# Kernel tuning notes

Measured on AMD Instinct MI355X. Metric: run time of the kernel, lower is better.

Reference implementation:

```python
import jax, jax.numpy as jnp
import numpy as np

# hparams (SpeechSplit-style, scaled up)
MAX_LEN_SEQ = 2048
MAX_LEN_PAD = 2560
MIN_LEN_SEG = 19
MAX_LEN_SEG = 32
MAX_NUM_SEG = MAX_LEN_SEQ // MIN_LEN_SEG + 1  # 108
B = 32
D = 80
S = MAX_LEN_SEG * 2  # 64 candidate interp positions per segment
N = B * MAX_NUM_SEG  # 3456


def setup_inputs() -> dict:
    key = jax.random.key(0)
    k1, k2, k3, k4 = jax.random.split(key, 4)
    x = jax.random.normal(k1, (B, MAX_LEN_PAD, D), dtype=jnp.float32)
    len_seq = jax.random.randint(k2, (B,), 0, MAX_LEN_SEQ, dtype=jnp.int32)
    scales_u = jax.random.uniform(k3, (N,), dtype=jnp.float32)  # uniform [0,1); +0.5 inside reference
    len_seg_raw = jax.random.randint(k4, (N, 1), 0, MAX_LEN_SEG - MIN_LEN_SEG, dtype=jnp.int32)
    return {"x": x, "len_seq": len_seq, "scales_u": scales_u, "len_seg_raw": len_seg_raw}


def reference(x, len_seq, scales_u, len_seg_raw):
    b, tx, d = x.shape
    # per-segment scaled time indices
    idx = jnp.arange(S, dtype=jnp.float32)[None, :]                     # (1, S)
    scales = scales_u + 0.5                                             # (N,) in [0.5, 1.5)
    idx_scaled = idx / scales[:, None]                                  # (N, S)
    idx_fl = jnp.floor(idx_scaled)
    lam = idx_scaled - idx_fl                                           # lerp weight (N, S)
    len_seg = len_seg_raw + MIN_LEN_SEG                                 # (N, 1) int
    idx_mask = idx_fl < (len_seg.astype(jnp.float32) - 1.0)             # within this segment
    # cumulative segment offsets per batch row
    offset = jnp.cumsum(len_seg.reshape(b, MAX_NUM_SEG), axis=-1)
    offset = jnp.pad(offset[:, :-1], ((0, 0), (1, 0))).reshape(-1, 1)   # (N, 1)
    idx_org = idx_fl + offset.astype(jnp.float32)                       # absolute source frame
    len_seq_rp = jnp.repeat(len_seq, MAX_NUM_SEG)                       # (N,)
    mask = idx_mask & (idx_org < (len_seq_rp - 1).astype(jnp.float32)[:, None])  # (N, S)

    mask_f = mask.reshape(-1)                                           # (N*S,)
    pos = jnp.cumsum(mask_f.astype(jnp.int32)) - 1                      # compacted position per element
    total = mask_f.astype(jnp.int32).sum()                              # total compacted rows

    # gather floor/ceil frames (index_1 = batch row of each flattened element)
    elem_batch = (jnp.arange(N * S, dtype=jnp.int32) // (MAX_NUM_SEG * S))
    i_fl = jnp.clip(idx_org.reshape(-1).astype(jnp.int32), 0, tx - 2)   # masked elems always in-range
    y_fl = x[elem_batch, i_fl]                                          # (N*S, D)
    y_cl = x[elem_batch, i_fl + 1]                                      # (N*S, D)
    lam_f = lam.reshape(-1, 1)
    y = (1.0 - lam_f) * y_fl + lam_f * y_cl                             # linear interp

    # boolean compaction via scatter into fixed-size buffer (masked-out rows dropped)
    write_pos = jnp.where(mask_f, pos, N * S)
    buf = jnp.zeros((N * S, d), x.dtype).at[write_pos].set(y, mode='drop')

    # reshape compacted stream to (b, total//b, d), trim/pad to MAX_LEN_PAD
    rows = total // b
    t = jnp.arange(MAX_LEN_PAD)
    gidx = jnp.arange(b)[:, None] * rows + t[None, :]                   # (b, MAX_LEN_PAD)
    valid = t[None, :] < rows
    out = jnp.where(valid[..., None], buf[jnp.clip(gidx, 0, N * S - 1)], 0.0)
    return out
```

## Files before the change

kernel.cpp:

```cpp
#include <hip/hip_runtime.h>
#include <hip/hip_bf16.h>

#define MAX_LEN_PAD 2560
#define MIN_LEN_SEG 19
#define MAX_NUM_SEG 108
#define B_ROWS      32
#define S_CAND      64
#define N_SEG       3456

#define WS_META      0
#define WS_SEGSTART  16
#define WS_SEGOFF    3504
#define WS_TABLE     8192

__global__ __launch_bounds__(576) void k1_scan(
    const int* __restrict__ len_seq, const float* __restrict__ scales_u,
    const int* __restrict__ len_seg_raw, int* __restrict__ ws)
{
    __shared__ int s_part[16];
    __shared__ int s_rowcum[B_ROWS];

    const int tid  = threadIdx.x;
    const int lane = tid & 63;
    const int wave = tid >> 6;
    const int brow = tid / 18;

    int v[6]; float sc[6];
    int sum = 0;
    #pragma unroll
    for (int j = 0; j < 6; ++j) {
        int k = tid * 6 + j;
        v[j]  = len_seg_raw[k] + MIN_LEN_SEG;
        sc[j] = scales_u[k];
        sum  += v[j];
    }

    int incl = sum;
    #pragma unroll
    for (int d = 1; d < 64; d <<= 1) {
        int o = __shfl_up(incl, d, 64);
        if (lane >= d) incl += o;
    }
    if (lane == 63) s_part[wave] = incl;
    __syncthreads();
    if (tid == 0) {
        int run = 0;
        #pragma unroll
        for (int w = 0; w < 9; ++w) { int p = s_part[w]; s_part[w] = run; run += p; }
    }
    __syncthreads();
    const int gbase = s_part[wave] + incl - sum;
    if (tid % 18 == 0) s_rowcum[brow] = gbase;
    __syncthreads();

    const int ls = len_seq[brow];
    const int rowc = s_rowcum[brow];
    int cnt[6]; int csum = 0;
    int* seg_off = ws + WS_SEGOFF;
    {
        int run = gbase;
        #pragma unroll
        for (int j = 0; j < 6; ++j) {
            int off = run - rowc;
            seg_off[tid * 6 + j] = off;
            run += v[j];
            float scale = sc[j] + 0.5f;
            int T = v[j] - 1;
            int lim = ls - 1 - off;
            if (lim < T) T = lim;
            float Tf = (float)T;
            int lo = 0, hi = S_CAND;
            while (lo < hi) {
                int mid = (lo + hi) >> 1;
                if (floorf((float)mid / scale) < Tf) lo = mid + 1; else hi = mid;
            }
            cnt[j] = lo; csum += lo;
        }
    }

    int cincl = csum;
    #pragma unroll
    for (int d = 1; d < 64; d <<= 1) {
        int o = __shfl_up(cincl, d, 64);
        if (lane >= d) cincl += o;
    }
    if (lane == 63) s_part[wave] = cincl;
    __syncthreads();
    if (tid == 0) {
        int run = 0;
        #pragma unroll
        for (int w = 0; w < 9; ++w) { int p = s_part[w]; s_part[w] = run; run += p; }
        int total = run;
        ws[WS_SEGSTART + N_SEG] = total;
        int rows = total / B_ROWS;
        int M = rows < MAX_LEN_PAD ? rows : MAX_LEN_PAD;
        ws[WS_META + 0] = rows;
        ws[WS_META + 1] = M;
    }
    __syncthreads();
    {
        int run = s_part[wave] + cincl - csum;
        int* seg_start = ws + WS_SEGSTART;
        #pragma unroll
        for (int j = 0; j < 6; ++j) { seg_start[tid * 6 + j] = run; run += cnt[j]; }
    }
}

__global__ __launch_bounds__(512) void k2_table(
    const float* __restrict__ scales_u, int* __restrict__ ws)
{
    const int n = blockIdx.x * 8 + (threadIdx.x >> 6);
    const int s = threadIdx.x & 63;
    const int rows = ws[WS_META + 0];
    if (rows <= 0) return;

    const int* seg_start = ws + WS_SEGSTART;
    int s0  = seg_start[n];
    int cnt = seg_start[n + 1] - s0;
    if (s >= cnt) return;

    float scale = scales_u[n] + 0.5f;
    int off = ws[WS_SEGOFF + n];
    int g = s0 + s;
    int b_out = g / rows;
    int t = g - b_out * rows;
    if (b_out < B_ROWS && t < MAX_LEN_PAD) {
        float q  = (float)s / scale;
        float fi = floorf(q);
        float lam = q - fi;
        int i_fl = (int)fi + off;
        if (i_fl > MAX_LEN_PAD - 2) i_fl = MAX_LEN_PAD - 2;
        int src = (n / MAX_NUM_SEG) * MAX_LEN_PAD + i_fl;
        ((int2*)(ws + WS_TABLE))[b_out * MAX_LEN_PAD + t] =
            make_int2(src, __float_as_int(lam));
    }
}

__global__ __launch_bounds__(640) void k3_gather(
    const float* __restrict__ x, const int* __restrict__ ws,
    float* __restrict__ out)
{
    const int M = ws[WS_META + 1];
    int flat = blockIdx.x * 640 + threadIdx.x;
    int r  = flat / 20;
    int q4 = flat - r * 20;
    int t  = r % MAX_LEN_PAD;

    float4 res = make_float4(0.f, 0.f, 0.f, 0.f);
    if (t < M) {
        int2 e = ((const int2*)(ws + WS_TABLE))[r];
        int src = e.x;
        float lam = __int_as_float(e.y);
        const float4* x4 = (const float4*)x;
        float4 a = x4[src * 20 + q4];
        float4 c = x4[src * 20 + 20 + q4];
        float om = 1.0f - lam;
        res.x = om * a.x + lam * c.x;
        res.y = om * a.y + lam * c.y;
        res.z = om * a.z + lam * c.z;
        res.w = om * a.w + lam * c.w;
    }
    ((float4*)out)[flat] = res;
}

extern "C" void kernel_launch(void* const* d_in, const int* in_sizes, int n_in,
                              void* d_out, int out_size, void* d_ws, size_t ws_size,
                              hipStream_t stream) {
    (void)in_sizes; (void)n_in; (void)out_size; (void)ws_size;
    const float* x           = (const float*)d_in[0];
    const int*   len_seq     = (const int*)d_in[1];
    const float* scales_u    = (const float*)d_in[2];
    const int*   len_seg_raw = (const int*)d_in[3];
    float* out = (float*)d_out;
    int*   ws  = (int*)d_ws;

    k1_scan<<<1, 576, 0, stream>>>(len_seq, scales_u, len_seg_raw, ws);
    k2_table<<<432, 512, 0, stream>>>(scales_u, ws);
    k3_gather<<<2560, 640, 0, stream>>>(x, ws, out);
}
```

Before: 90.87 us.

## Fuse interpolation table construction into single-block scan kernel

Merges the table-building kernel into the scan kernel. The scan runs in one 1024-thread block that keeps segment starts, offsets and scales in shared memory, then writes the gather table in 16-element chunks per thread. This removes a kernel launch and the workspace round-trip for segment metadata. The cost is that the whole table is written by a single workgroup, which limits parallelism and memory throughput for that phase.

```diff
diff --git a/kernel.cpp b/kernel.cpp
--- a/kernel.cpp
+++ b/kernel.cpp
@@ -8,31 +8,35 @@
 #define S_CAND      64
 #define N_SEG       3456
 
-#define WS_META      0
-#define WS_SEGSTART  16
-#define WS_SEGOFF    3504
-#define WS_TABLE     8192
+#define WS_META   0
+#define WS_TABLE  8192
 
-__global__ __launch_bounds__(576) void k1_scan(
+__global__ __launch_bounds__(1024) void k1_all(
     const int* __restrict__ len_seq, const float* __restrict__ scales_u,
     const int* __restrict__ len_seg_raw, int* __restrict__ ws)
 {
-    __shared__ int s_part[16];
-    __shared__ int s_rowcum[B_ROWS];
+    __shared__ int   s_part[16];
+    __shared__ int   s_rowcum[B_ROWS];
+    __shared__ int   s_misc[2];
+    __shared__ int   s_start[N_SEG + 1];
+    __shared__ int   s_off[N_SEG];
+    __shared__ float s_scale[N_SEG];
 
-    const int tid  = threadIdx.x;
-    const int lane = tid & 63;
-    const int wave = tid >> 6;
-    const int brow = tid / 18;
+    const int tid    = threadIdx.x;
+    const int lane   = tid & 63;
+    const int wave   = tid >> 6;
+    const bool active = tid < N_SEG / 6;
+    const int brow   = tid / 18;
 
-    int v[6]; float sc[6];
-    int sum = 0;
-    #pragma unroll
-    for (int j = 0; j < 6; ++j) {
-        int k = tid * 6 + j;
-        v[j]  = len_seg_raw[k] + MIN_LEN_SEG;
-        sc[j] = scales_u[k];
-        sum  += v[j];
+    int v[6]; float sc[6]; int sum = 0;
+    if (active) {
+        #pragma unroll
+        for (int j = 0; j < 6; ++j) {
+            int k = tid * 6 + j;
+            v[j]  = len_seg_raw[k] + MIN_LEN_SEG;
+            sc[j] = scales_u[k];
+            sum  += v[j];
+        }
     }
 
     int incl = sum;
@@ -46,23 +50,22 @@
     if (tid == 0) {
         int run = 0;
         #pragma unroll
-        for (int w = 0; w < 9; ++w) { int p = s_part[w]; s_part[w] = run; run += p; }
+        for (int w = 0; w < 16; ++w) { int p = s_part[w]; s_part[w] = run; run += p; }
     }
     __syncthreads();
     const int gbase = s_part[wave] + incl - sum;
-    if (tid % 18 == 0) s_rowcum[brow] = gbase;
+    if (active && (tid % 18 == 0)) s_rowcum[brow] = gbase;
     __syncthreads();
 
-    const int ls = len_seq[brow];
-    const int rowc = s_rowcum[brow];
-    int cnt[6]; int csum = 0;
-    int* seg_off = ws + WS_SEGOFF;
-    {
+    int cnt[6]; int csum = 0; int offv[6];
+    if (active) {
+        const int ls   = len_seq[brow];
+        const int rowc = s_rowcum[brow];
         int run = gbase;
         #pragma unroll
         for (int j = 0; j < 6; ++j) {
             int off = run - rowc;
-            seg_off[tid * 6 + j] = off;
+            offv[j] = off;
             run += v[j];
             float scale = sc[j] + 0.5f;
             int T = v[j] - 1;
@@ -89,50 +92,57 @@
     if (tid == 0) {
         int run = 0;
         #pragma unroll
-        for (int w = 0; w < 9; ++w) { int p = s_part[w]; s_part[w] = run; run += p; }
+        for (int w = 0; w < 16; ++w) { int p = s_part[w]; s_part[w] = run; run += p; }
         int total = run;
-        ws[WS_SEGSTART + N_SEG] = total;
         int rows = total / B_ROWS;
         int M = rows < MAX_LEN_PAD ? rows : MAX_LEN_PAD;
+        s_misc[0] = rows; s_misc[1] = M;
         ws[WS_META + 0] = rows;
         ws[WS_META + 1] = M;
+        s_start[N_SEG] = total;
     }
     __syncthreads();
-    {
+    if (active) {
         int run = s_part[wave] + cincl - csum;
-        int* seg_start = ws + WS_SEGSTART;
         #pragma unroll
-        for (int j = 0; j < 6; ++j) { seg_start[tid * 6 + j] = run; run += cnt[j]; }
+        for (int j = 0; j < 6; ++j) {
+            int k = tid * 6 + j;
+            s_start[k] = run; run += cnt[j];
+            s_off[k]   = offv[j];
+            s_scale[k] = sc[j];
+        }
     }
-}
+    __syncthreads();
 
-__global__ __launch_bounds__(512) void k2_table(
-    const float* __restrict__ scales_u, int* __restrict__ ws)
-{
-    const int n = blockIdx.x * 8 + (threadIdx.x >> 6);
-    const int s = threadIdx.x & 63;
-    const int rows = ws[WS_META + 0];
-    if (rows <= 0) return;
-
-    const int* seg_start = ws + WS_SEGSTART;
-    int s0  = seg_start[n];
-    int cnt = seg_start[n + 1] - s0;
-    if (s >= cnt) return;
-
-    float scale = scales_u[n] + 0.5f;
-    int off = ws[WS_SEGOFF + n];
-    int g = s0 + s;
-    int b_out = g / rows;
-    int t = g - b_out * rows;
-    if (b_out < B_ROWS && t < MAX_LEN_PAD) {
-        float q  = (float)s / scale;
-        float fi = floorf(q);
-        float lam = q - fi;
-        int i_fl = (int)fi + off;
-        if (i_fl > MAX_LEN_PAD - 2) i_fl = MAX_LEN_PAD - 2;
-        int src = (n / MAX_NUM_SEG) * MAX_LEN_PAD + i_fl;
-        ((int2*)(ws + WS_TABLE))[b_out * MAX_LEN_PAD + t] =
-            make_int2(src, __float_as_int(lam));
+    const int rows = s_misc[0];
+    if (rows > 0) {
+        int2* table = (int2*)(ws + WS_TABLE);
+        for (int u = tid; u < N_SEG * 4; u += 1024) {
+            int n  = u >> 2;
+            int c0 = (u & 3) << 4;
+            int st = s_start[n];
+            int cn = s_start[n + 1] - st;
+            if (c0 >= cn) continue;
+            int smax = cn < c0 + 16 ? cn : c0 + 16;
+            float scale = s_scale[n] + 0.5f;
+            int off     = s_off[n];
+            int srcbase = (n / MAX_NUM_SEG) * MAX_LEN_PAD;
+            int g  = st + c0;
+            int bo = g / rows;
+            int t  = g - bo * rows;
+            for (int s = c0; s < smax; ++s) {
+                if (bo < B_ROWS && t < MAX_LEN_PAD) {
+                    float q  = (float)s / scale;
+                    float fi = floorf(q);
+                    float lam = q - fi;
+                    int i_fl = (int)fi + off;
+                    if (i_fl > MAX_LEN_PAD - 2) i_fl = MAX_LEN_PAD - 2;
+                    table[bo * MAX_LEN_PAD + t] =
+                        make_int2(srcbase + i_fl, __float_as_int(lam));
+                }
+                if (++t >= rows) { t = 0; ++bo; }
+            }
+        }
     }
 }
 
@@ -174,7 +184,6 @@
     float* out = (float*)d_out;
     int*   ws  = (int*)d_ws;
 
-    k1_scan<<<1, 576, 0, stream>>>(len_seq, scales_u, len_seg_raw, ws);
-    k2_table<<<432, 512, 0, stream>>>(scales_u, ws);
+    k1_all<<<1, 1024, 0, stream>>>(len_seq, scales_u, len_seg_raw, ws);
     k3_gather<<<2560, 640, 0, stream>>>(x, ws, out);
 }
```

Result: slower. 115.0 us (+26.6%).
